# Kernel tuning notes

Hardware: AMD Instinct MI355X
Metric: run time of the kernel (lower is better)

Reference implementation:

```python
import jax, jax.numpy as jnp
import numpy as np

N_AGENTS = 8192
OBS_DIM = 520
EMBED = 64
HID = 128
N_ACT = 6


def setup_inputs() -> dict:
    key = jax.random.key(0)
    ks = jax.random.split(key, 16)
    s = 0.05  # small init scale for numerical stability
    return {
        "obs": jax.random.normal(ks[0], (N_AGENTS, OBS_DIM), jnp.float32),
        "beliefs": jax.random.normal(ks[1], (N_AGENTS, HID), jnp.float32),
        "W1": jax.random.normal(ks[2], (OBS_DIM, EMBED), jnp.float32) * s,
        "b1": jnp.zeros((EMBED,), jnp.float32),
        "W2": jax.random.normal(ks[3], (EMBED, EMBED), jnp.float32) * s,
        "b2": jnp.zeros((EMBED,), jnp.float32),
        "Wb": jax.random.normal(ks[4], (HID, EMBED), jnp.float32) * s,
        "bb": jnp.zeros((EMBED,), jnp.float32),
        "Wg": jax.random.normal(ks[5], (2 * EMBED, HID), jnp.float32) * s,
        "bg": jnp.zeros((HID,), jnp.float32),
        "Wir": jax.random.normal(ks[6], (HID, HID), jnp.float32) * s,
        "Wiz": jax.random.normal(ks[7], (HID, HID), jnp.float32) * s,
        "Win": jax.random.normal(ks[8], (HID, HID), jnp.float32) * s,
        "Whr": jax.random.normal(ks[9], (HID, HID), jnp.float32) * s,
        "bhr": jnp.zeros((HID,), jnp.float32),
        "Whz": jax.random.normal(ks[10], (HID, HID), jnp.float32) * s,
        "bhz": jnp.zeros((HID,), jnp.float32),
        "Whn": jax.random.normal(ks[11], (HID, HID), jnp.float32) * s,
        "bhn": jnp.zeros((HID,), jnp.float32),
        "Wout": jax.random.normal(ks[12], (HID, N_ACT), jnp.float32) * s,
        "bout": jnp.zeros((N_ACT,), jnp.float32),
    }


def reference(obs, beliefs, W1, b1, W2, b2, Wb, bb, Wg, bg,
              Wir, Wiz, Win, Whr, bhr, Whz, bhz, Whn, bhn, Wout, bout):
    n_agents = obs.shape[0]
    # obs MLP: Dense -> relu -> Dense -> relu  [A, EMBED]
    h_obs = jax.nn.relu(obs @ W1 + b1)
    h_obs = jax.nn.relu(h_obs @ W2 + b2)
    # belief projection [A, EMBED]
    bp = beliefs @ Wb + bb
    # self-attention over beliefs with diagonal masked out
    attn_logits = (bp @ bp.T) / jnp.sqrt(jnp.asarray(EMBED, bp.dtype))
    attn_logits = attn_logits + jnp.eye(n_agents, dtype=bp.dtype) * (-1e8)
    attn_weights = jax.nn.softmax(attn_logits, axis=-1)
    contexts = attn_weights @ bp  # [A, EMBED]
    # GRU input projection [A, HID]
    gru_in = jnp.concatenate([h_obs, contexts], axis=-1) @ Wg + bg
    # flax GRUCell (input denses bias-free, hidden denses biased)
    r = jax.nn.sigmoid(gru_in @ Wir + beliefs @ Whr + bhr)
    z = jax.nn.sigmoid(gru_in @ Wiz + beliefs @ Whz + bhz)
    n = jnp.tanh(gru_in @ Win + r * (beliefs @ Whn + bhn))
    new_beliefs = (1.0 - z) * n + z * beliefs
    logits = new_beliefs @ Wout + bout
    return (logits, new_beliefs)
```

## Files before the change

kernel.cpp:

```cpp
#include <hip/hip_runtime.h>

#define A_N 8192
#define OBS_D 520
#define EMB 64
#define HID 128
#define NACT 6
#define SPLIT 16

typedef short bf16x8 __attribute__((ext_vector_type(8)));
typedef _Float16 half8 __attribute__((ext_vector_type(8)));
typedef float f32x4 __attribute__((ext_vector_type(4)));
typedef unsigned short u16;
typedef unsigned int u32;

#define MFMA_BF(a,b,c) __builtin_amdgcn_mfma_f32_16x16x32_bf16(a,b,c,0,0,0)
#define MFMA_FH(a,b,c) __builtin_amdgcn_mfma_f32_16x16x32_f16(a,b,c,0,0,0)

__device__ inline u32 fbits(float f){ union{float f; u32 u;}v; v.f=f; return v.u; }
__device__ inline float fval(u32 u){ union{u32 u; float f;}v; v.u=u; return v.f; }
__device__ inline u16 f2bf(float f){ u32 u=fbits(f); u += 0x7fffu + ((u>>16)&1u); return (u16)(u>>16); }
__device__ inline u32 pk_bf(float pe, float po){
  return __builtin_amdgcn_perm(fbits(po), fbits(pe), 0x07060302u);
}
__device__ inline float sigmoidf_fast(float x){
  x = fminf(fmaxf(x, -30.f), 30.f);
  return 1.f / (1.f + __expf(-x));
}
__device__ inline float tanhf_fast(float x){
  x = fminf(fmaxf(x, -15.f), 15.f);
  float e = __expf(-2.f*x);
  return (1.f - e) / (1.f + e);
}

#define EXP2C 0.18033688011112042f

__global__ __launch_bounds__(256) void kPrep2(
    const float* __restrict__ Wg, const float* __restrict__ Wir,
    const float* __restrict__ Wiz, const float* __restrict__ Win,
    const float* __restrict__ Whr, const float* __restrict__ Whz,
    const float* __restrict__ Whn, const float* __restrict__ W1,
    const float* __restrict__ W2, const float* __restrict__ Wb,
    const float* __restrict__ beliefs, const float* __restrict__ bb,
    _Float16* __restrict__ WT, _Float16* __restrict__ W1T,
    _Float16* __restrict__ W2T, u16* __restrict__ bp, u16* __restrict__ bpT)
{
  __shared__ float tile[64][65];
  __shared__ u16 WbL[64][136];
  const int t = threadIdx.x, b = blockIdx.x;

  if (b < 38) {
    const float* src; int k0, c0, srcStride, kValid;
    if (b < 28) {
      const int mi = b >> 2, tl = b & 3;
      src = mi==0?Wg: mi==1?Wir: mi==2?Wiz: mi==3?Win: mi==4?Whr: mi==5?Whz: Whn;
      k0 = (tl >> 1) * 64; c0 = (tl & 1) * 64; srcStride = 128; kValid = 128;
    } else if (b < 37) {
      src = W1; k0 = (b - 28) * 64; c0 = 0; srcStride = 64; kValid = OBS_D;
    } else {
      src = W2; k0 = 0; c0 = 0; srcStride = 64; kValid = 64;
    }
    #pragma unroll
    for (int i = 0; i < 16; i++) {
      const int idx = i * 256 + t;
      const int rr = idx >> 6, cc = idx & 63;
      tile[rr][cc] = (k0 + rr < kValid) ? src[(size_t)(k0 + rr) * srcStride + c0 + cc] : 0.f;
    }
    __syncthreads();
    if (b < 28) {
      const int mi = b >> 2;
      _Float16* dst = WT + (size_t)mi * 16384;
      #pragma unroll
      for (int i = 0; i < 16; i++) {
        const int idx = i * 256 + t;
        const int rr = idx >> 6, cc = idx & 63;
        dst[(size_t)(c0 + rr) * 128 + k0 + cc] = (_Float16)tile[cc][rr];
      }
    } else if (b < 37) {
      #pragma unroll
      for (int i = 0; i < 16; i++) {
        const int idx = i * 256 + t;
        const int rr = idx >> 6, cc = idx & 63;
        if (k0 + cc < 544)
          W1T[(size_t)rr * 544 + k0 + cc] = (_Float16)tile[cc][rr];
      }
    } else {
      #pragma unroll
      for (int i = 0; i < 16; i++) {
        const int idx = i * 256 + t;
        const int rr = idx >> 6, cc = idx & 63;
        W2T[(size_t)rr * 64 + cc] = (_Float16)tile[cc][rr];
      }
    }
  } else {
    const int lane = t & 63, wid = t >> 6;
    const int m = lane & 15, quad = lane >> 4;
    const int r0 = (b - 38) * 64 + wid * 16;

    #pragma unroll
    for (int i = 0; i < 8; i++) {
      const int i4 = i * 256 + t;
      float4 w4 = ((const float4*)Wb)[i4];
      const int k = i4 >> 4, c = (i4 & 15) * 4;
      WbL[c+0][k] = f2bf(w4.x); WbL[c+1][k] = f2bf(w4.y);
      WbL[c+2][k] = f2bf(w4.z); WbL[c+3][k] = f2bf(w4.w);
    }
    __syncthreads();

    f32x4 acc[4];
    #pragma unroll
    for (int ct = 0; ct < 4; ct++) acc[ct] = (f32x4){0.f,0.f,0.f,0.f};
    #pragma unroll
    for (int s = 0; s < 4; s++) {
      const int k0 = s*32;
      const float* ap = beliefs + (size_t)(r0+m)*HID + k0 + quad*8;
      float4 a0 = *(const float4*)ap;
      float4 a1 = *(const float4*)(ap + 4);
      union { u16 e[8]; bf16x8 v; } av;
      av.e[0]=f2bf(a0.x); av.e[1]=f2bf(a0.y); av.e[2]=f2bf(a0.z); av.e[3]=f2bf(a0.w);
      av.e[4]=f2bf(a1.x); av.e[5]=f2bf(a1.y); av.e[6]=f2bf(a1.z); av.e[7]=f2bf(a1.w);
      #pragma unroll
      for (int ct = 0; ct < 4; ct++) {
        bf16x8 bw = *(const bf16x8*)&WbL[ct*16+m][k0 + quad*8];
        acc[ct] = MFMA_BF(av.v, bw, acc[ct]);
      }
    }
    #pragma unroll
    for (int ct = 0; ct < 4; ct++) {
      const int col = ct*16 + m;
      const float bbv = bb[col];
      u16 e[4];
      #pragma unroll
      for (int r = 0; r < 4; r++) e[r] = f2bf(acc[ct][r] + bbv);
      #pragma unroll
      for (int r = 0; r < 4; r++)
        bp[(size_t)(r0 + quad*4 + r)*EMB + col] = e[r];
      uint2 pkv;
      pkv.x = (u32)e[0] | ((u32)e[1] << 16);
      pkv.y = (u32)e[2] | ((u32)e[3] << 16);
      *(uint2*)(bpT + (size_t)col*A_N + r0 + quad*4) = pkv;
    }
  }
}

__global__ __launch_bounds__(256) void kM(
    const u16* __restrict__ bp, const u16* __restrict__ bpT,
    u16* __restrict__ ctxp, float* __restrict__ sums,
    const float* __restrict__ obs, const _Float16* __restrict__ W1T,
    const float* __restrict__ b1, const _Float16* __restrict__ W2T,
    const float* __restrict__ b2, _Float16* __restrict__ h2f)
{
  __shared__ __align__(16) u16 P[4][4][16 * 72];
  const int lane = threadIdx.x & 63;
  const int wid  = threadIdx.x >> 6;
  const int m = lane & 15, quad = lane >> 4;

  if (blockIdx.x >= 128) {
    const int w = (blockIdx.x - 128) * 4 + wid;
    const int split = w >> 7;
    const int qt = w & 127;
    const int q0 = qt * 64;

    bf16x8 qa[4][2];
    #pragma unroll
    for (int f = 0; f < 4; f++) {
      const u16* qr = bp + (size_t)(q0 + f*16 + m)*EMB + quad*8;
      qa[f][0] = *(const bf16x8*)(qr);
      qa[f][1] = *(const bf16x8*)(qr + 32);
    }
    f32x4 oacc[4][4];
    #pragma unroll
    for (int f = 0; f < 4; f++)
      #pragma unroll
      for (int d = 0; d < 4; d++) oacc[f][d] = (f32x4){0.f,0.f,0.f,0.f};
    float rowsum[4] = {0.f, 0.f, 0.f, 0.f};

    const int kbeg = split * (A_N / SPLIT);
    const int kend = kbeg + (A_N / SPLIT);

    for (int k0 = kbeg; k0 < kend; k0 += 64) {
      #pragma unroll
      for (int jt = 0; jt < 4; jt++) {
        const u16* kr = bp + (size_t)(k0 + jt*16 + m)*EMB + quad*8;
        const bf16x8 kb0 = *(const bf16x8*)(kr);
        const bf16x8 kb1 = *(const bf16x8*)(kr + 32);
        #pragma unroll
        for (int f = 0; f < 4; f++) {
          f32x4 s = (f32x4){0.f,0.f,0.f,0.f};
          s = MFMA_BF(kb0, qa[f][0], s);
          s = MFMA_BF(kb1, qa[f][1], s);
          float p0 = __builtin_amdgcn_exp2f(s[0]*EXP2C);
          float p1 = __builtin_amdgcn_exp2f(s[1]*EXP2C);
          float p2 = __builtin_amdgcn_exp2f(s[2]*EXP2C);
          float p3 = __builtin_amdgcn_exp2f(s[3]*EXP2C);
          if ((k0 + jt*16) == (q0 + f*16)) {
            const int jl = quad*4;
            if (jl + 0 == m) p0 = 0.f;
            if (jl + 1 == m) p1 = 0.f;
            if (jl + 2 == m) p2 = 0.f;
            if (jl + 3 == m) p3 = 0.f;
          }
          rowsum[f] += (p0 + p1) + (p2 + p3);
          uint2 pkv; pkv.x = pk_bf(p0, p1); pkv.y = pk_bf(p2, p3);
          *(uint2*)&P[wid][f][m*72 + jt*16 + quad*4] = pkv;
        }
      }
      bf16x8 vb[4][2];
      #pragma unroll
      for (int dtt = 0; dtt < 4; dtt++) {
        const u16* vr = bpT + (size_t)(dtt*16+m)*A_N + k0 + quad*8;
        vb[dtt][0] = *(const bf16x8*)(vr);
        vb[dtt][1] = *(const bf16x8*)(vr + 32);
      }
      asm volatile("s_waitcnt lgkmcnt(0)" ::: "memory");
      #pragma unroll
      for (int f = 0; f < 4; f++) {
        const bf16x8 pa0 = *(const bf16x8*)&P[wid][f][m*72 + quad*8];
        const bf16x8 pa1 = *(const bf16x8*)&P[wid][f][m*72 + 32 + quad*8];
        #pragma unroll
        for (int dtt = 0; dtt < 4; dtt++) {
          oacc[f][dtt] = MFMA_BF(pa0, vb[dtt][0], oacc[f][dtt]);
          oacc[f][dtt] = MFMA_BF(pa1, vb[dtt][1], oacc[f][dtt]);
        }
      }
    }

    #pragma unroll
    for (int f = 0; f < 4; f++) {
      float v = rowsum[f];
      v += __shfl_xor(v, 16, 64);
      v += __shfl_xor(v, 32, 64);
      if (lane < 16)
        sums[(size_t)split*A_N + q0 + f*16 + lane] = v;
    }
    #pragma unroll
    for (int f = 0; f < 4; f++) {
      const size_t base = ((size_t)split*A_N + q0 + f*16) * EMB;
      #pragma unroll
      for (int dtt = 0; dtt < 4; dtt++)
        #pragma unroll
        for (int r = 0; r < 4; r++)
          ctxp[base + (size_t)(quad*4+r)*EMB + dtt*16 + m] = f2bf(oacc[f][dtt][r]);
    }
  } else {
    const int r0 = blockIdx.x * 64 + wid * 16;
    f32x4 oa[4];
    #pragma unroll
    for (int ct = 0; ct < 4; ct++) oa[ct] = (f32x4){0.f,0.f,0.f,0.f};

    for (int s = 0; s < 17; s++) {
      const int k0 = s * 32;
      union { _Float16 e[8]; half8 v; } af;
      if (s < 16) {
        const float* ap = obs + (size_t)(r0+m)*OBS_D + k0 + quad*8;
        float4 a0 = *(const float4*)ap;
        float4 a1 = *(const float4*)(ap + 4);
        af.e[0]=(_Float16)a0.x; af.e[1]=(_Float16)a0.y; af.e[2]=(_Float16)a0.z; af.e[3]=(_Float16)a0.w;
        af.e[4]=(_Float16)a1.x; af.e[5]=(_Float16)a1.y; af.e[6]=(_Float16)a1.z; af.e[7]=(_Float16)a1.w;
      } else {
        #pragma unroll
        for (int j = 0; j < 8; j++) af.e[j] = (_Float16)0.f;
        if (quad == 0) {
          const float* ap = obs + (size_t)(r0+m)*OBS_D + 512;
          float4 a0 = *(const float4*)ap;
          float4 a1 = *(const float4*)(ap + 4);
          af.e[0]=(_Float16)a0.x; af.e[1]=(_Float16)a0.y; af.e[2]=(_Float16)a0.z; af.e[3]=(_Float16)a0.w;
          af.e[4]=(_Float16)a1.x; af.e[5]=(_Float16)a1.y; af.e[6]=(_Float16)a1.z; af.e[7]=(_Float16)a1.w;
        }
      }
      #pragma unroll
      for (int ct = 0; ct < 4; ct++) {
        half8 bw = *(const half8*)(W1T + (size_t)(ct*16+m)*544 + k0 + quad*8);
        oa[ct] = MFMA_FH(af.v, bw, oa[ct]);
      }
    }
    _Float16* H1 = (_Float16*)&P[wid][0][0];
    #pragma unroll
    for (int ct = 0; ct < 4; ct++) {
      const float b1v = b1[ct*16 + m];
      #pragma unroll
      for (int r = 0; r < 4; r++) {
        float v = fmaxf(oa[ct][r] + b1v, 0.f);
        H1[(quad*4+r)*72 + ct*16 + m] = (_Float16)v;
      }
    }
    __syncthreads();
    f32x4 ob[4];
    #pragma unroll
    for (int ct = 0; ct < 4; ct++) ob[ct] = (f32x4){0.f,0.f,0.f,0.f};
    #pragma unroll
    for (int s2 = 0; s2 < 2; s2++) {
      half8 ah = *(const half8*)(H1 + m*72 + s2*32 + quad*8);
      #pragma unroll
      for (int ct = 0; ct < 4; ct++) {
        half8 bw = *(const half8*)(W2T + (size_t)(ct*16+m)*64 + s2*32 + quad*8);
        ob[ct] = MFMA_FH(ah, bw, ob[ct]);
      }
    }
    #pragma unroll
    for (int ct = 0; ct < 4; ct++) {
      const float b2v = b2[ct*16 + m];
      #pragma unroll
      for (int r = 0; r < 4; r++) {
        float v = fmaxf(ob[ct][r] + b2v, 0.f);
        h2f[(size_t)(r0 + quad*4 + r)*EMB + ct*16 + m] = (_Float16)v;
      }
    }
  }
}

__global__ __launch_bounds__(256) void k3_gru(
    const float* __restrict__ beliefs, const _Float16* __restrict__ h2f,
    const u16* __restrict__ ctxp, const float* __restrict__ sums,
    const _Float16* __restrict__ WT,
    const float* __restrict__ bg, const float* __restrict__ bhr,
    const float* __restrict__ bhz, const float* __restrict__ bhn,
    const float* __restrict__ Wout, const float* __restrict__ bout,
    float* __restrict__ out)
{
  __shared__ __align__(16) _Float16 xf[32][136];
  __shared__ __align__(16) _Float16 belf[32][136];
  __shared__ __align__(16) _Float16 gruf[32][136];
  __shared__ float invs[32];
  const int t = threadIdx.x;
  const int lane = t & 63, wid = t >> 6;
  const int m = lane & 15, quad = lane >> 4;
  const int r0 = blockIdx.x * 32;

  #pragma unroll
  for (int i = 0; i < 2; i++) {
    const int idx = i*256 + t;
    const int row = idx >> 4, seg = idx & 15;
    const float* bpR = beliefs + (size_t)(r0+row)*HID + seg*8;
    float4 a0 = *(const float4*)bpR;
    float4 a1 = *(const float4*)(bpR + 4);
    union { _Float16 e[8]; half8 v; } hb;
    hb.e[0]=(_Float16)a0.x; hb.e[1]=(_Float16)a0.y; hb.e[2]=(_Float16)a0.z; hb.e[3]=(_Float16)a0.w;
    hb.e[4]=(_Float16)a1.x; hb.e[5]=(_Float16)a1.y; hb.e[6]=(_Float16)a1.z; hb.e[7]=(_Float16)a1.w;
    *(half8*)&belf[row][seg*8] = hb.v;
  }
  const int crow = t >> 3, cg = t & 7;
  {
    half8 hv = *(const half8*)(h2f + (size_t)(r0+crow)*EMB + cg*8);
    *(half8*)&xf[crow][cg*8] = hv;
  }
  float ca[8];
  #pragma unroll
  for (int d = 0; d < 8; d++) ca[d] = 0.f;
  #pragma unroll
  for (int sp = 0; sp < SPLIT; sp++) {
    uint4 u = *(const uint4*)(ctxp + ((size_t)sp*A_N + r0 + crow)*EMB + cg*8);
    ca[0] += fval(u.x << 16); ca[1] += fval(u.x & 0xffff0000u);
    ca[2] += fval(u.y << 16); ca[3] += fval(u.y & 0xffff0000u);
    ca[4] += fval(u.z << 16); ca[5] += fval(u.z & 0xffff0000u);
    ca[6] += fval(u.w << 16); ca[7] += fval(u.w & 0xffff0000u);
  }
  if (t < 32) {
    float ss = 0.f;
    #pragma unroll
    for (int sp = 0; sp < SPLIT; sp++) ss += sums[(size_t)sp*A_N + r0 + t];
    invs[t] = 1.f / ss;
  }
  __syncthreads();
  {
    const float iv = invs[crow];
    union { _Float16 e[8]; half8 v; } hc;
    #pragma unroll
    for (int d = 0; d < 8; d++) hc.e[d] = (_Float16)(ca[d] * iv);
    *(half8*)&xf[crow][64 + cg*8] = hc.v;
  }
  __syncthreads();

  f32x4 g[2][2];
  #pragma unroll
  for (int rt = 0; rt < 2; rt++)
    #pragma unroll
    for (int ci = 0; ci < 2; ci++) g[rt][ci] = (f32x4){0.f,0.f,0.f,0.f};
  #pragma unroll
  for (int s = 0; s < 4; s++) {
    half8 bw0 = *(const half8*)(WT + (size_t)((wid*2+0)*16+m)*128 + s*32 + quad*8);
    half8 bw1 = *(const half8*)(WT + (size_t)((wid*2+1)*16+m)*128 + s*32 + quad*8);
    #pragma unroll
    for (int rt = 0; rt < 2; rt++) {
      half8 ax = *(const half8*)&xf[rt*16 + m][s*32 + quad*8];
      g[rt][0] = MFMA_FH(ax, bw0, g[rt][0]);
      g[rt][1] = MFMA_FH(ax, bw1, g[rt][1]);
    }
  }
  #pragma unroll
  for (int rt = 0; rt < 2; rt++)
    #pragma unroll
    for (int ci = 0; ci < 2; ci++) {
      const int col = (wid*2+ci)*16 + m;
      const float bgv = bg[col];
      #pragma unroll
      for (int r = 0; r < 4; r++)
        gruf[rt*16 + quad*4 + r][col] = (_Float16)(g[rt][ci][r] + bgv);
    }
  __syncthreads();

  f32x4 RV[2][2], ZV[2][2];
  #pragma unroll
  for (int gidx = 0; gidx < 3; gidx++) {
    const _Float16* WiTg = WT + (size_t)(1+gidx)*16384;
    const _Float16* WhTg = WT + (size_t)(4+gidx)*16384;
    f32x4 gi[2][2], gh[2][2];
    #pragma unroll
    for (int rt = 0; rt < 2; rt++)
      #pragma unroll
      for (int ci = 0; ci < 2; ci++) {
        gi[rt][ci] = (f32x4){0.f,0.f,0.f,0.f};
        gh[rt][ci] = (f32x4){0.f,0.f,0.f,0.f};
      }
    #pragma unroll
    for (int s = 0; s < 4; s++) {
      half8 bi0 = *(const half8*)(WiTg + (size_t)((wid*2+0)*16+m)*128 + s*32 + quad*8);
      half8 bi1 = *(const half8*)(WiTg + (size_t)((wid*2+1)*16+m)*128 + s*32 + quad*8);
      half8 bh0 = *(const half8*)(WhTg + (size_t)((wid*2+0)*16+m)*128 + s*32 + quad*8);
      half8 bh1 = *(const half8*)(WhTg + (size_t)((wid*2+1)*16+m)*128 + s*32 + quad*8);
      #pragma unroll
      for (int rt = 0; rt < 2; rt++) {
        half8 ag = *(const half8*)&gruf[rt*16 + m][s*32 + quad*8];
        half8 ab = *(const half8*)&belf[rt*16 + m][s*32 + quad*8];
        gi[rt][0] = MFMA_FH(ag, bi0, gi[rt][0]);
        gi[rt][1] = MFMA_FH(ag, bi1, gi[rt][1]);
        gh[rt][0] = MFMA_FH(ab, bh0, gh[rt][0]);
        gh[rt][1] = MFMA_FH(ab, bh1, gh[rt][1]);
      }
    }
    if (gidx == 0) {
      #pragma unroll
      for (int rt = 0; rt < 2; rt++)
        #pragma unroll
        for (int ci = 0; ci < 2; ci++) {
          const float bv = bhr[(wid*2+ci)*16 + m];
          #pragma unroll
          for (int r = 0; r < 4; r++)
            RV[rt][ci][r] = sigmoidf_fast(gi[rt][ci][r] + gh[rt][ci][r] + bv);
        }
    } else if (gidx == 1) {
      #pragma unroll
      for (int rt = 0; rt < 2; rt++)
        #pragma unroll
        for (int ci = 0; ci < 2; ci++) {
          const float bv = bhz[(wid*2+ci)*16 + m];
          #pragma unroll
          for (int r = 0; r < 4; r++)
            ZV[rt][ci][r] = sigmoidf_fast(gi[rt][ci][r] + gh[rt][ci][r] + bv);
        }
    } else {
      #pragma unroll
      for (int rt = 0; rt < 2; rt++)
        #pragma unroll
        for (int ci = 0; ci < 2; ci++) {
          const int col = (wid*2+ci)*16 + m;
          const float bv = bhn[col];
          #pragma unroll
          for (int r = 0; r < 4; r++) {
            const int row = rt*16 + quad*4 + r;
            float bel = (float)belf[row][col];
            float pre = gi[rt][ci][r] + RV[rt][ci][r] * (gh[rt][ci][r] + bv);
            float nv = tanhf_fast(pre);
            float nb = (1.f - ZV[rt][ci][r]) * nv + ZV[rt][ci][r] * bel;
            xf[row][col] = (_Float16)nb;
          }
        }
    }
  }
  __syncthreads();

  float* woutL = (float*)&gruf[0][0];
  if (t < 192) ((float4*)woutL)[t] = ((const float4*)Wout)[t];
  #pragma unroll
  for (int i = 0; i < 4; i++) {
    const int lin = i*256 + t;
    const int row = lin >> 5, c4 = (lin & 31) * 4;
    float4 o;
    o.x = (float)xf[row][c4+0]; o.y = (float)xf[row][c4+1];
    o.z = (float)xf[row][c4+2]; o.w = (float)xf[row][c4+3];
    *(float4*)&out[(size_t)NACT*A_N + (size_t)(r0+row)*HID + c4] = o;
  }
  __syncthreads();

  if (t < 32*NACT) {
    const int row = t / NACT, c = t % NACT;
    float a = bout[c];
    #pragma unroll 8
    for (int k = 0; k < HID; k++)
      a += (float)xf[row][k] * woutL[k*NACT + c];
    out[(size_t)(r0+row)*NACT + c] = a;
  }
}

extern "C" void kernel_launch(void* const* d_in, const int* in_sizes, int n_in,
                              void* d_out, int out_size, void* d_ws, size_t ws_size,
                              hipStream_t stream) {
  const float* obs     = (const float*)d_in[0];
  const float* beliefs = (const float*)d_in[1];
  const float* W1      = (const float*)d_in[2];
  const float* b1      = (const float*)d_in[3];
  const float* W2      = (const float*)d_in[4];
  const float* b2      = (const float*)d_in[5];
  const float* Wb      = (const float*)d_in[6];
  const float* bb      = (const float*)d_in[7];
  const float* Wg      = (const float*)d_in[8];
  const float* bg      = (const float*)d_in[9];
  const float* Wir     = (const float*)d_in[10];
  const float* Wiz     = (const float*)d_in[11];
  const float* Win     = (const float*)d_in[12];
  const float* Whr     = (const float*)d_in[13];
  const float* bhr     = (const float*)d_in[14];
  const float* Whz     = (const float*)d_in[15];
  const float* bhz     = (const float*)d_in[16];
  const float* Whn     = (const float*)d_in[17];
  const float* bhn     = (const float*)d_in[18];
  const float* Wout    = (const float*)d_in[19];
  const float* bout    = (const float*)d_in[20];
  float* out = (float*)d_out;

  char* ws = (char*)d_ws;
  _Float16* h2f  = (_Float16*)(ws);
  u16*      bp   = (u16*)(ws + 1048576);
  u16*      bpT  = (u16*)(ws + 2097152);
  u16*      ctxp = (u16*)(ws + 3145728);
  float*    sums = (float*)(ws + 19922944);
  _Float16* WT   = (_Float16*)(ws + 20447232);
  _Float16* W1T  = (_Float16*)(ws + 20676608);
  _Float16* W2T  = (_Float16*)(ws + 20746240);

  hipLaunchKernelGGL(kPrep2, dim3(166), dim3(256), 0, stream,
                     Wg, Wir, Wiz, Win, Whr, Whz, Whn, W1, W2, Wb, beliefs, bb,
                     WT, W1T, W2T, bp, bpT);
  hipLaunchKernelGGL(kM, dim3(640), dim3(256), 0, stream,
                     bp, bpT, ctxp, sums, obs, W1T, b1, W2T, b2, h2f);
  hipLaunchKernelGGL(k3_gru, dim3(256), dim3(256), 0, stream,
                     beliefs, h2f, ctxp, sums, WT, bg, bhr, bhz, bhn, Wout, bout, out);
}
```

Baseline: 167.4 us.

## Share K/V tiles across block waves via double-buffered LDS staging

Attention blocks now give all four waves the same key split and adjacent query tiles. Each 64-row K tile and V^T tile is loaded once per block into double-buffered LDS, with a register prefetch of the next tile, instead of every wave reading K and V from global memory on its own. The P buffer shrinks to two f-tiles per wave and is processed in two halves to fit the LDS budget. This cuts redundant global/L2 traffic but adds block-wide barriers and LDS read pressure.

New measurement: 155.3 us. 1.08x faster.

```diff
diff --git a/kernel.cpp b/kernel.cpp
--- a/kernel.cpp
+++ b/kernel.cpp
@@ -149,21 +149,25 @@
     const float* __restrict__ b1, const _Float16* __restrict__ W2T,
     const float* __restrict__ b2, _Float16* __restrict__ h2f)
 {
-  __shared__ __align__(16) u16 P[4][4][16 * 72];
-  const int lane = threadIdx.x & 63;
-  const int wid  = threadIdx.x >> 6;
+  __shared__ __align__(16) u16 KT[2][64*72];
+  __shared__ __align__(16) u16 VTl[2][64*72];
+  __shared__ __align__(16) u16 P2[4][2][16*72];
+  const int tid = threadIdx.x;
+  const int lane = tid & 63;
+  const int wid  = tid >> 6;
   const int m = lane & 15, quad = lane >> 4;
 
   if (blockIdx.x >= 128) {
-    const int w = (blockIdx.x - 128) * 4 + wid;
-    const int split = w >> 7;
-    const int qt = w & 127;
-    const int q0 = qt * 64;
+    const int ab = blockIdx.x - 128;
+    const int split = ab >> 5;
+    const int qb = ab & 31;
+    const int q0w = qb * 256 + wid * 64;
+    const int kbeg = split * (A_N / SPLIT);
 
     bf16x8 qa[4][2];
     #pragma unroll
     for (int f = 0; f < 4; f++) {
-      const u16* qr = bp + (size_t)(q0 + f*16 + m)*EMB + quad*8;
+      const u16* qr = bp + (size_t)(q0w + f*16 + m)*EMB + quad*8;
       qa[f][0] = *(const bf16x8*)(qr);
       qa[f][1] = *(const bf16x8*)(qr + 32);
     }
@@ -174,53 +178,80 @@
       for (int d = 0; d < 4; d++) oacc[f][d] = (f32x4){0.f,0.f,0.f,0.f};
     float rowsum[4] = {0.f, 0.f, 0.f, 0.f};
 
-    const int kbeg = split * (A_N / SPLIT);
-    const int kend = kbeg + (A_N / SPLIT);
-
-    for (int k0 = kbeg; k0 < kend; k0 += 64) {
-      #pragma unroll
-      for (int jt = 0; jt < 4; jt++) {
-        const u16* kr = bp + (size_t)(k0 + jt*16 + m)*EMB + quad*8;
-        const bf16x8 kb0 = *(const bf16x8*)(kr);
-        const bf16x8 kb1 = *(const bf16x8*)(kr + 32);
-        #pragma unroll
-        for (int f = 0; f < 4; f++) {
-          f32x4 s = (f32x4){0.f,0.f,0.f,0.f};
-          s = MFMA_BF(kb0, qa[f][0], s);
-          s = MFMA_BF(kb1, qa[f][1], s);
-          float p0 = __builtin_amdgcn_exp2f(s[0]*EXP2C);
-          float p1 = __builtin_amdgcn_exp2f(s[1]*EXP2C);
-          float p2 = __builtin_amdgcn_exp2f(s[2]*EXP2C);
-          float p3 = __builtin_amdgcn_exp2f(s[3]*EXP2C);
-          if ((k0 + jt*16) == (q0 + f*16)) {
-            const int jl = quad*4;
-            if (jl + 0 == m) p0 = 0.f;
-            if (jl + 1 == m) p1 = 0.f;
-            if (jl + 2 == m) p2 = 0.f;
-            if (jl + 3 == m) p3 = 0.f;
+    uint4 kreg[2], vreg[2];
+    const int srow0 = tid >> 3, seg = tid & 7;
+    const int srow1 = (256 + tid) >> 3;
+
+    kreg[0] = *(const uint4*)(bp + (size_t)(kbeg + srow0)*EMB + seg*8);
+    kreg[1] = *(const uint4*)(bp + (size_t)(kbeg + srow1)*EMB + seg*8);
+    vreg[0] = *(const uint4*)(bpT + (size_t)srow0*A_N + kbeg + seg*8);
+    vreg[1] = *(const uint4*)(bpT + (size_t)srow1*A_N + kbeg + seg*8);
+    *(uint4*)&KT[0][srow0*72 + seg*8] = kreg[0];
+    *(uint4*)&KT[0][srow1*72 + seg*8] = kreg[1];
+    *(uint4*)&VTl[0][srow0*72 + seg*8] = vreg[0];
+    *(uint4*)&VTl[0][srow1*72 + seg*8] = vreg[1];
+    __syncthreads();
+
+    for (int tt = 0; tt < 8; tt++) {
+      const int k0 = kbeg + tt*64;
+      const int cur = tt & 1;
+      if (tt < 7) {
+        const int kn = k0 + 64;
+        kreg[0] = *(const uint4*)(bp + (size_t)(kn + srow0)*EMB + seg*8);
+        kreg[1] = *(const uint4*)(bp + (size_t)(kn + srow1)*EMB + seg*8);
+        vreg[0] = *(const uint4*)(bpT + (size_t)srow0*A_N + kn + seg*8);
+        vreg[1] = *(const uint4*)(bpT + (size_t)srow1*A_N + kn + seg*8);
+      }
+      #pragma unroll
+      for (int h = 0; h < 2; h++) {
+        #pragma unroll
+        for (int jt = 0; jt < 4; jt++) {
+          const bf16x8 kb0 = *(const bf16x8*)&KT[cur][(jt*16+m)*72 + quad*8];
+          const bf16x8 kb1 = *(const bf16x8*)&KT[cur][(jt*16+m)*72 + 32 + quad*8];
+          #pragma unroll
+          for (int fi = 0; fi < 2; fi++) {
+            const int f = h*2 + fi;
+            f32x4 s = (f32x4){0.f,0.f,0.f,0.f};
+            s = MFMA_BF(kb0, qa[f][0], s);
+            s = MFMA_BF(kb1, qa[f][1], s);
+            float p0 = __builtin_amdgcn_exp2f(s[0]*EXP2C);
+            float p1 = __builtin_amdgcn_exp2f(s[1]*EXP2C);
+            float p2 = __builtin_amdgcn_exp2f(s[2]*EXP2C);
+            float p3 = __builtin_amdgcn_exp2f(s[3]*EXP2C);
+            if ((k0 + jt*16) == (q0w + f*16)) {
+              const int jl = quad*4;
+              if (jl + 0 == m) p0 = 0.f;
+              if (jl + 1 == m) p1 = 0.f;
+              if (jl + 2 == m) p2 = 0.f;
+              if (jl + 3 == m) p3 = 0.f;
+            }
+            rowsum[f] += (p0 + p1) + (p2 + p3);
+            uint2 pkv; pkv.x = pk_bf(p0, p1); pkv.y = pk_bf(p2, p3);
+            *(uint2*)&P2[wid][fi][m*72 + jt*16 + quad*4] = pkv;
           }
-          rowsum[f] += (p0 + p1) + (p2 + p3);
-          uint2 pkv; pkv.x = pk_bf(p0, p1); pkv.y = pk_bf(p2, p3);
-          *(uint2*)&P[wid][f][m*72 + jt*16 + quad*4] = pkv;
         }
-      }
-      bf16x8 vb[4][2];
-      #pragma unroll
-      for (int dtt = 0; dtt < 4; dtt++) {
-        const u16* vr = bpT + (size_t)(dtt*16+m)*A_N + k0 + quad*8;
-        vb[dtt][0] = *(const bf16x8*)(vr);
-        vb[dtt][1] = *(const bf16x8*)(vr + 32);
-      }
-      asm volatile("s_waitcnt lgkmcnt(0)" ::: "memory");
-      #pragma unroll
-      for (int f = 0; f < 4; f++) {
-        const bf16x8 pa0 = *(const bf16x8*)&P[wid][f][m*72 + quad*8];
-        const bf16x8 pa1 = *(const bf16x8*)&P[wid][f][m*72 + 32 + quad*8];
-        #pragma unroll
-        for (int dtt = 0; dtt < 4; dtt++) {
-          oacc[f][dtt] = MFMA_BF(pa0, vb[dtt][0], oacc[f][dtt]);
-          oacc[f][dtt] = MFMA_BF(pa1, vb[dtt][1], oacc[f][dtt]);
+        asm volatile("s_waitcnt lgkmcnt(0)" ::: "memory");
+        #pragma unroll
+        for (int fi = 0; fi < 2; fi++) {
+          const int f = h*2 + fi;
+          const bf16x8 pa0 = *(const bf16x8*)&P2[wid][fi][m*72 + quad*8];
+          const bf16x8 pa1 = *(const bf16x8*)&P2[wid][fi][m*72 + 32 + quad*8];
+          #pragma unroll
+          for (int dtt = 0; dtt < 4; dtt++) {
+            const bf16x8 vb0 = *(const bf16x8*)&VTl[cur][(dtt*16+m)*72 + quad*8];
+            const bf16x8 vb1 = *(const bf16x8*)&VTl[cur][(dtt*16+m)*72 + 32 + quad*8];
+            oacc[f][dtt] = MFMA_BF(pa0, vb0, oacc[f][dtt]);
+            oacc[f][dtt] = MFMA_BF(pa1, vb1, oacc[f][dtt]);
+          }
         }
+      }
+      if (tt < 7) {
+        const int nxt = cur ^ 1;
+        *(uint4*)&KT[nxt][srow0*72 + seg*8] = kreg[0];
+        *(uint4*)&KT[nxt][srow1*72 + seg*8] = kreg[1];
+        *(uint4*)&VTl[nxt][srow0*72 + seg*8] = vreg[0];
+        *(uint4*)&VTl[nxt][srow1*72 + seg*8] = vreg[1];
+        __syncthreads();
       }
     }
 
@@ -230,11 +261,11 @@
       v += __shfl_xor(v, 16, 64);
       v += __shfl_xor(v, 32, 64);
       if (lane < 16)
-        sums[(size_t)split*A_N + q0 + f*16 + lane] = v;
+        sums[(size_t)split*A_N + q0w + f*16 + lane] = v;
     }
     #pragma unroll
     for (int f = 0; f < 4; f++) {
-      const size_t base = ((size_t)split*A_N + q0 + f*16) * EMB;
+      const size_t base = ((size_t)split*A_N + q0w + f*16) * EMB;
       #pragma unroll
       for (int dtt = 0; dtt < 4; dtt++)
         #pragma unroll
@@ -273,7 +304,7 @@
         oa[ct] = MFMA_FH(af.v, bw, oa[ct]);
       }
     }
-    _Float16* H1 = (_Float16*)&P[wid][0][0];
+    _Float16* H1 = (_Float16*)&P2[wid][0][0];
     #pragma unroll
     for (int ct = 0; ct < 4; ct++) {
       const float b1v = b1[ct*16 + m];
```
